# Kernel optimization log

Measured on AMD Instinct MI355X. Metric: run time of the kernel, lower is better.

## Reference

```python
import jax, jax.numpy as jnp
import numpy as np

E = 21   # numParticipants (experts)
D = 128  # input features (hardcoded Linear(128,16))
H = 16   # hidden
N = 262144  # rows


def setup_inputs() -> dict:
    key = jax.random.key(0)
    ks = jax.random.split(key, 6)
    x = jax.random.normal(ks[0], (N, D), dtype=jnp.float32)
    sid = jax.random.randint(ks[1], (N,), 0, E)
    s1 = 1.0 / np.sqrt(D)
    W1 = jax.random.uniform(ks[2], (E, D, H), jnp.float32, -s1, s1)
    b1 = jax.random.uniform(ks[3], (E, H), jnp.float32, -s1, s1)
    s2 = 1.0 / np.sqrt(H)
    W2 = jax.random.uniform(ks[4], (E, H), jnp.float32, -s2, s2)  # Linear(16,1) weight, squeezed
    b2 = jax.random.uniform(ks[5], (E,), jnp.float32, -s2, s2)
    return {"x": x, "sid": sid, "W1": W1, "b1": b1, "W2": W2, "b2": b2}


def reference(x, sid, W1, b1, W2, b2):
    # Per-row expert MLP: h = relu(x @ W1[sid] + b1[sid]); y = relu(h . W2[sid] + b2[sid]).
    # Dropout(0.5) is identity in eval mode. Vectorized routing: compute first layer for
    # all 21 tiny experts ([N,E,H] ~ 350MB), then select the routed expert per row.
    h_all = jax.nn.relu(jnp.einsum('nd,edh->neh', x, W1) + b1[None, :, :])  # [N,E,H]
    h = jnp.take_along_axis(h_all, sid[:, None, None], axis=1)[:, 0, :]      # [N,H]
    y = jax.nn.relu(jnp.einsum('nh,nh->n', h, W2[sid]) + b2[sid])            # [N]
    return y[:, None]  # [N,1]
```

## Files before the change

### kernel.cpp

```cpp
#include <hip/hip_runtime.h>

#define N_ROWS 262144
#define DIM    128
#define HID    16
#define NEXP   21
#define NSEG   (N_ROWS / 64 + NEXP)
#define NBLK1  256
#define RPB    (N_ROWS / NBLK1)
#define RPT    (RPB / 256)

__global__ __launch_bounds__(256) void k_hist(const int* __restrict__ sid,
                                              int* __restrict__ counts,
                                              int* __restrict__ blockBase) {
    __shared__ int lh[NEXP];
    int t = threadIdx.x;
    if (t < NEXP) lh[t] = 0;
    __syncthreads();
    int base = blockIdx.x * RPB + t;
#pragma unroll
    for (int r = 0; r < RPT; r++) {
        atomicAdd(&lh[sid[base + r * 256]], 1);
    }
    __syncthreads();
    if (t < NEXP) blockBase[blockIdx.x * NEXP + t] = atomicAdd(&counts[t], lh[t]);
}

__global__ __launch_bounds__(256) void k_scatter(const int* __restrict__ sid,
                                                 const int* __restrict__ counts,
                                                 const int* __restrict__ blockBase,
                                                 int* __restrict__ buckets) {
    __shared__ int sbase[NEXP];
    __shared__ int lcur[NEXP];
    int t = threadIdx.x;
    if (t == 0) {
        int acc = 0;
        for (int e = 0; e < NEXP; e++) {
            sbase[e] = acc + blockBase[blockIdx.x * NEXP + e];
            acc += ((counts[e] + 63) >> 6) << 6;
        }
    }
    if (t < NEXP) lcur[t] = 0;
    __syncthreads();
    int base = blockIdx.x * RPB + t;
#pragma unroll
    for (int r = 0; r < RPT; r++) {
        int row = base + r * 256;
        int e = sid[row];
        int lp = atomicAdd(&lcur[e], 1);
        buckets[sbase[e] + lp] = row | (e << 24);
    }
}

__global__ __launch_bounds__(256, 4) void k_main(const float* __restrict__ x,
                                                 const float* __restrict__ W1,
                                                 const float* __restrict__ b1,
                                                 const float* __restrict__ W2,
                                                 const float* __restrict__ b2,
                                                 const int* __restrict__ buckets,
                                                 float* __restrict__ out) {
    int seg = blockIdx.x * 4 + (threadIdx.x >> 6);
    if (seg >= NSEG) return;
    int lane = threadIdx.x & 63;
    int ent = buckets[seg * 64 + lane];
    if (__ballot(ent >= 0) == 0ULL) return;
    int e = __builtin_amdgcn_readfirstlane(ent) >> 24;
    int row = ent & 0x00FFFFFF;
    int vrow = (ent >= 0) ? row : 0;

    const float* __restrict__ w1 = W1 + e * (DIM * HID);
    const float4* __restrict__ xr = (const float4*)(x + (size_t)vrow * DIM);

    float h[HID];
#pragma unroll
    for (int j = 0; j < HID; j++) h[j] = b1[e * HID + j];

    float4 v0 = xr[0], v1 = xr[1], v2 = xr[2], v3 = xr[3];

#pragma unroll
    for (int b = 0; b < 8; b++) {
        float4 n0, n1, n2, n3;
        if (b < 7) {
            n0 = xr[b * 4 + 4];
            n1 = xr[b * 4 + 5];
            n2 = xr[b * 4 + 6];
            n3 = xr[b * 4 + 7];
        }
        const int k0 = b * 16;
        const float xv[16] = {v0.x, v0.y, v0.z, v0.w, v1.x, v1.y, v1.z, v1.w,
                              v2.x, v2.y, v2.z, v2.w, v3.x, v3.y, v3.z, v3.w};
#pragma unroll
        for (int t = 0; t < 16; t++) {
#pragma unroll
            for (int j = 0; j < HID; j++)
                h[j] = fmaf(xv[t], w1[(k0 + t) * HID + j], h[j]);
        }
        if (b < 7) { v0 = n0; v1 = n1; v2 = n2; v3 = n3; }
    }

    float acc = b2[e];
#pragma unroll
    for (int j = 0; j < HID; j++) acc = fmaf(fmaxf(h[j], 0.0f), W2[e * HID + j], acc);
    if (ent >= 0) out[row] = fmaxf(acc, 0.0f);
}

__global__ __launch_bounds__(256) void k_naive(const float* __restrict__ x,
                                               const int* __restrict__ sid,
                                               const float* __restrict__ W1,
                                               const float* __restrict__ b1,
                                               const float* __restrict__ W2,
                                               const float* __restrict__ b2,
                                               float* __restrict__ out) {
    int row = blockIdx.x * 256 + threadIdx.x;
    if (row >= N_ROWS) return;
    int e = sid[row];
    const float* w1 = W1 + e * (DIM * HID);
    const float* xr = x + (size_t)row * DIM;
    float h[HID];
#pragma unroll
    for (int j = 0; j < HID; j++) h[j] = b1[e * HID + j];
    for (int k = 0; k < DIM; k++) {
        float xk = xr[k];
#pragma unroll
        for (int j = 0; j < HID; j++) h[j] = fmaf(xk, w1[k * HID + j], h[j]);
    }
    float acc = b2[e];
#pragma unroll
    for (int j = 0; j < HID; j++) acc = fmaf(fmaxf(h[j], 0.0f), W2[e * HID + j], acc);
    out[row] = fmaxf(acc, 0.0f);
}

extern "C" void kernel_launch(void* const* d_in, const int* in_sizes, int n_in,
                              void* d_out, int out_size, void* d_ws, size_t ws_size,
                              hipStream_t stream) {
    const float* x   = (const float*)d_in[0];
    const int*   sid = (const int*)d_in[1];
    const float* W1  = (const float*)d_in[2];
    const float* b1  = (const float*)d_in[3];
    const float* W2  = (const float*)d_in[4];
    const float* b2  = (const float*)d_in[5];
    float* out = (float*)d_out;

    const size_t bucketBytes = (size_t)NSEG * 64 * sizeof(int);
    const size_t countBytes  = 32 * sizeof(int);
    const size_t bbBytes     = (size_t)NBLK1 * NEXP * sizeof(int);
    const size_t need = bucketBytes + countBytes + bbBytes;

    if (ws_size < need) {
        k_naive<<<(N_ROWS + 255) / 256, 256, 0, stream>>>(x, sid, W1, b1, W2, b2, out);
        return;
    }

    char* ws = (char*)d_ws;
    int* buckets   = (int*)ws;
    int* counts    = (int*)(ws + bucketBytes);
    int* blockBase = (int*)(ws + bucketBytes + countBytes);

    hipMemsetAsync(buckets, 0xFF, bucketBytes, stream);
    hipMemsetAsync(counts, 0, countBytes, stream);
    k_hist<<<NBLK1, 256, 0, stream>>>(sid, counts, blockBase);
    k_scatter<<<NBLK1, 256, 0, stream>>>(sid, counts, blockBase, buckets);
    k_main<<<(NSEG + 3) / 4, 256, 0, stream>>>(x, W1, b1, W2, b2, buckets, out);
}
```

Before: 236.1 us.

## Stage x rows into LDS with coalesced global_load_lds before per-row MLP

Replaces per-lane strided float4 loads of each routed row with cooperative 16-byte global_load_lds transfers, where eight lanes fetch contiguous 128-byte chunks of a row into a padded per-wave LDS buffer. Each lane then reads its own row from LDS in four quarter steps. This aims to improve global memory coalescing for the gathered rows. In exchange it adds LDS usage and full waitcnt barriers that serialize loads and compute, dropping the previous register prefetch overlap.

Measured after the change: 232.7 us. About the same (-1.4%).

```diff
diff --git a/kernel.cpp b/kernel.cpp
--- a/kernel.cpp
+++ b/kernel.cpp
@@ -1,4 +1,5 @@
 #include <hip/hip_runtime.h>
+#include <stdint.h>
 
 #define N_ROWS 262144
 #define DIM    128
@@ -8,6 +9,10 @@
 #define NBLK1  256
 #define RPB    (N_ROWS / NBLK1)
 #define RPT    (RPB / 256)
+
+#define PADB     1040
+#define WAVE_LDS (8 * PADB)
+#define BLK_LDS  (4 * WAVE_LDS)
 
 __global__ __launch_bounds__(256) void k_hist(const int* __restrict__ sid,
                                               int* __restrict__ counts,
@@ -51,50 +56,67 @@
     }
 }
 
-__global__ __launch_bounds__(256, 4) void k_main(const float* __restrict__ x,
-                                                 const float* __restrict__ W1,
-                                                 const float* __restrict__ b1,
-                                                 const float* __restrict__ W2,
-                                                 const float* __restrict__ b2,
-                                                 const int* __restrict__ buckets,
-                                                 float* __restrict__ out) {
-    int seg = blockIdx.x * 4 + (threadIdx.x >> 6);
+typedef __attribute__((address_space(1))) const uint32_t gu32;
+typedef __attribute__((address_space(3))) uint32_t lu32;
+
+__device__ __forceinline__ void stage16(const float* gp, char* lp) {
+    __builtin_amdgcn_global_load_lds((gu32*)(uintptr_t)gp,
+                                     (lu32*)(uintptr_t)lp, 16, 0, 0);
+}
+
+__global__ __launch_bounds__(256, 4) void k_main3(const float* __restrict__ x,
+                                                  const float* __restrict__ W1,
+                                                  const float* __restrict__ b1,
+                                                  const float* __restrict__ W2,
+                                                  const float* __restrict__ b2,
+                                                  const int* __restrict__ buckets,
+                                                  float* __restrict__ out) {
+    extern __shared__ char smem[];
+    const int seg = blockIdx.x * 4 + (threadIdx.x >> 6);
     if (seg >= NSEG) return;
-    int lane = threadIdx.x & 63;
+    const int lane = threadIdx.x & 63;
+    char* waveLds = smem + (threadIdx.x >> 6) * WAVE_LDS;
+
     int ent = buckets[seg * 64 + lane];
     if (__ballot(ent >= 0) == 0ULL) return;
-    int e = __builtin_amdgcn_readfirstlane(ent) >> 24;
-    int row = ent & 0x00FFFFFF;
-    int vrow = (ent >= 0) ? row : 0;
+    const int e = __builtin_amdgcn_readfirstlane(ent) >> 24;
+    const int row = ent & 0x00FFFFFF;
+    const int vrow = (ent >= 0) ? row : 0;
+
+    int rg[8];
+#pragma unroll
+    for (int g = 0; g < 8; g++) rg[g] = __shfl(vrow, g * 8 + (lane >> 3), 64);
+    const int c8 = lane & 7;
 
     const float* __restrict__ w1 = W1 + e * (DIM * HID);
-    const float4* __restrict__ xr = (const float4*)(x + (size_t)vrow * DIM);
-
     float h[HID];
 #pragma unroll
     for (int j = 0; j < HID; j++) h[j] = b1[e * HID + j];
 
-    float4 v0 = xr[0], v1 = xr[1], v2 = xr[2], v3 = xr[3];
+    const char* rb = waveLds + (lane >> 3) * PADB + (lane & 7) * 128;
 
 #pragma unroll
-    for (int b = 0; b < 8; b++) {
-        float4 n0, n1, n2, n3;
-        if (b < 7) {
-            n0 = xr[b * 4 + 4];
-            n1 = xr[b * 4 + 5];
-            n2 = xr[b * 4 + 6];
-            n3 = xr[b * 4 + 7];
+    for (int q = 0; q < 4; q++) {
+        __builtin_amdgcn_s_waitcnt(0);
+#pragma unroll
+        for (int g = 0; g < 8; g++) {
+            const float* gp = x + (size_t)rg[g] * DIM + q * 32 + c8 * 4;
+            stage16(gp, waveLds + g * PADB + lane * 16);
         }
-        const int k0 = b * 16;
-        const float xv[16] = {v0.x, v0.y, v0.z, v0.w, v1.x, v1.y, v1.z, v1.w,
-                              v2.x, v2.y, v2.z, v2.w, v3.x, v3.y, v3.z, v3.w};
+        __builtin_amdgcn_s_waitcnt(0);
 #pragma unroll
-        for (int t = 0; t < 16; t++) {
+        for (int m = 0; m < 8; m++) {
+            const float4 xv = *(const float4*)(rb + m * 16);
+            const int k0 = (q * 8 + m) * 4;
 #pragma unroll
-            for (int j = 0; j < HID; j++)
-                h[j] = fmaf(xv[t], w1[(k0 + t) * HID + j], h[j]);
+            for (int j = 0; j < HID; j++) h[j] = fmaf(xv.x, w1[(k0 + 0) * HID + j], h[j]);
+#pragma unroll
+            for (int j = 0; j < HID; j++) h[j] = fmaf(xv.y, w1[(k0 + 1) * HID + j], h[j]);
+#pragma unroll
+            for (int j = 0; j < HID; j++) h[j] = fmaf(xv.z, w1[(k0 + 2) * HID + j], h[j]);
+#pragma unroll
+            for (int j = 0; j < HID; j++) h[j] = fmaf(xv.w, w1[(k0 + 3) * HID + j], h[j]);
         }
-        if (b < 7) { v0 = n0; v1 = n1; v2 = n2; v3 = n3; }
     }
 
     float acc = b2[e];
@@ -159,5 +181,5 @@
     hipMemsetAsync(counts, 0, countBytes, stream);
     k_hist<<<NBLK1, 256, 0, stream>>>(sid, counts, blockBase);
     k_scatter<<<NBLK1, 256, 0, stream>>>(sid, counts, blockBase, buckets);
-    k_main<<<(NSEG + 3) / 4, 256, 0, stream>>>(x, W1, b1, W2, b2, buckets, out);
+    k_main3<<<(NSEG + 3) / 4, 256, BLK_LDS, stream>>>(x, W1, b1, W2, b2, buckets, out);
 }
```
